# Kernel optimization log

Measured on AMD Instinct MI355X. Metric: run time of the kernel, lower is better.

Reference implementation:

```python
import jax, jax.numpy as jnp
import numpy as np

WINDOW = 127          # odd
W = (WINDOW - 1) // 2 # 63 half-window
Q_CH = WINDOW + 1     # 128 query chunk
K_CH = WINDOW * 2     # 254 key chunk


def _compl_mod(m, n):
    return int(n * int(np.ceil(m / n)) - m)


def setup_inputs() -> dict:
    key = jax.random.key(0)
    kq, kk, kv = jax.random.split(key, 3)
    B, L, NH, H = 4, 4096, 16, 64
    return {
        "q": jax.random.normal(kq, (B, L, NH, H), dtype=jnp.float32),
        "k": jax.random.normal(kk, (B, L, NH, H), dtype=jnp.float32),
        "v": jax.random.normal(kv, (B, L, NH, H), dtype=jnp.float32),
    }


def _build_mask(c, k_pad, dtype_bool=bool):
    # base band mask over one (q_ch, k_ch) block: True = masked out
    u = jnp.triu(jnp.ones((Q_CH, K_CH), dtype=bool))
    band = jnp.logical_and(u, jnp.flip(u, (0, 1)))
    base = ~band
    mask_left = base.at[:, :W].set(True)
    mask_right = base.at[:, K_CH - (W + k_pad):].set(True)
    if c > 1:
        mid = jnp.broadcast_to(base, (c - 2, Q_CH, K_CH)) if c > 2 else jnp.zeros((0, Q_CH, K_CH), bool)
        return jnp.concatenate([mask_left[None], mid, mask_right[None]], axis=0)
    return jnp.logical_or(mask_left, mask_right)[None]


def reference(q, k, v):
    b, s, nh, h = q.shape
    q = q * (h ** -0.5)

    q_pad = _compl_mod(s, Q_CH)
    k_pad = _compl_mod(s + 2 * W - K_CH, Q_CH)

    # chunk queries: (b, c, q_ch, nh, h)
    qp = jnp.pad(q, ((0, 0), (0, q_pad), (0, 0), (0, 0)))
    c = (s + q_pad) // Q_CH
    qw = qp.reshape(b, c, Q_CH, nh, h)

    # overlapping key/value windows via gather: (b, c, k_ch, nh, h)
    kp = jnp.pad(k, ((0, 0), (W, W + k_pad), (0, 0), (0, 0)))
    vp = jnp.pad(v, ((0, 0), (W, W + k_pad), (0, 0), (0, 0)))
    starts = np.arange(c) * Q_CH
    idx = starts[:, None] + np.arange(K_CH)[None, :]  # (c, k_ch)
    kw = kp[:, idx]
    vw = vp[:, idx]

    # block scores: (b, nh, c, q_ch, k_ch)
    A = jnp.einsum('bcqnh,bcknh->bncqk', qw, kw)

    mask = _build_mask(c, k_pad)  # (c, q_ch, k_ch)
    neg = -jnp.finfo(A.dtype).max
    A = jnp.where(mask[None, None], neg, A)
    A = jax.nn.softmax(A, axis=-1)

    z = jnp.einsum('bncqk,bcknh->bncqh', A, vw)  # (b, nh, c, q_ch, h)
    z = z.reshape(b, nh, c * Q_CH, h)[:, :, :s]
    return jnp.transpose(z, (0, 2, 1, 3))  # (b, s, nh, h)
```

## Files before the change

kernel.cpp:

```cpp
#include <hip/hip_runtime.h>


typedef _Float16 f16;
typedef _Float16 f16x2  __attribute__((ext_vector_type(2)));
typedef _Float16 f16x4  __attribute__((ext_vector_type(4)));
typedef _Float16 f16x8  __attribute__((ext_vector_type(8)));
typedef float    f32x16 __attribute__((ext_vector_type(16)));
typedef int      int4v  __attribute__((ext_vector_type(4)));

constexpr int NB = 4, L = 4096, NH = 16, H = 64;
constexpr int CQ = 128, NC = L / CQ, KW = 256, WR = 63;
constexpr int RS = NH * H;

constexpr int Q_OFF = 0;
constexpr int K_OFF = 16384;
constexpr int V_OFF = 49152;
constexpr int LDS_BYTES = 81920;

#define DEV static __device__ __forceinline__

DEV int iclamp(int x, int lo, int hi) { return x < lo ? lo : (x > hi ? hi : x); }

DEV float fexp2(float x) {
#if __has_builtin(__builtin_amdgcn_exp2f)
    return __builtin_amdgcn_exp2f(x);
#else
    return exp2f(x);
#endif
}

DEV int packh2(float a, float b) {
    f16x2 p; p.x = (f16)a; p.y = (f16)b;
    return __builtin_bit_cast(int, p);
}

DEV int rmaddr(int base, int r, int colb) {
    return base + r * 128 + (colb ^ ((r & 7) << 4));
}

DEV int vaddr(int h, int kb) {
    return V_OFF + ((h * 512 + kb) ^ ((((h & 7) ^ ((h >> 3) & 7))) << 4));
}

DEV int oaddr(int row, int col) {
    return (row * 64 + col) ^ ((row & 3) << 2);
}

DEV void swap_halves(int& a, int& b, int hi) {
    int pa = __shfl_xor(a, 32, 64);
    int pb = __shfl_xor(b, 32, 64);
    int na = hi ? pb : a;
    int nb = hi ? b  : pa;
    a = na; b = nb;
}

__global__ __launch_bounds__(512, 4)
void wattn_kernel(const float* __restrict__ q_, const float* __restrict__ k_,
                  const float* __restrict__ v_, float* __restrict__ o_)
{
    __shared__ alignas(16) char smem[LDS_BYTES];
    float* O_lds = (float*)smem;
    float* D_lds = (float*)(smem + 32768);

    const int bid = (int)blockIdx.x;
    const int wid = (bid & 7) * ((NB * NH * NC) / 8) + (bid >> 3);
    const int c = wid & (NC - 1);
    const int n = (wid >> 5) & (NH - 1);
    const int b = wid >> 9;

    const int t    = (int)threadIdx.x;
    const int lane = t & 63;
    const int w    = t >> 6;
    const int lq   = lane & 31;
    const int hi   = lane >> 5;
    const int qt   = w & 3;
    const int half = w >> 2;

    const int kg0 = c * CQ - WR;
    const size_t bn = ((size_t)b * L * NH + n) * H;
    const float qs = 0.125f * 1.44269504088896f;

    const int h4 = (t & 15) << 2;
    const int cb = h4 << 1;
    const int ru = t >> 4;

    {
        const float* qp = q_ + bn + (size_t)(c * CQ) * RS + h4;
        #pragma unroll
        for (int p = 0; p < 4; ++p) {
            int r = ru + p * 32;
            float4 x = *(const float4*)(qp + (size_t)r * RS);
            *(f16x4*)(smem + rmaddr(Q_OFF, r, cb)) =
                (f16x4){(f16)(x.x * qs), (f16)(x.y * qs), (f16)(x.z * qs), (f16)(x.w * qs)};
        }
    }
    #pragma unroll
    for (int p = 0; p < 8; ++p) {
        int r  = ru + p * 32;
        int kr = iclamp(kg0 + r, 0, L - 1);
        float4 x = *(const float4*)(k_ + bn + (size_t)kr * RS + h4);
        *(f16x4*)(smem + rmaddr(K_OFF, r, cb)) =
            (f16x4){(f16)x.x, (f16)x.y, (f16)x.z, (f16)x.w};
    }
    #pragma unroll
    for (int p = 0; p < 4; ++p) {
        int r0  = ru * 2 + p * 64;
        int kr0 = iclamp(kg0 + r0,     0, L - 1);
        int kr1 = iclamp(kg0 + r0 + 1, 0, L - 1);
        float4 v0 = *(const float4*)(v_ + bn + (size_t)kr0 * RS + h4);
        float4 v1 = *(const float4*)(v_ + bn + (size_t)kr1 * RS + h4);
        int kb = r0 * 2;
        *(f16x2*)(smem + vaddr(h4 + 0, kb)) = (f16x2){(f16)v0.x, (f16)v1.x};
        *(f16x2*)(smem + vaddr(h4 + 1, kb)) = (f16x2){(f16)v0.y, (f16)v1.y};
        *(f16x2*)(smem + vaddr(h4 + 2, kb)) = (f16x2){(f16)v0.z, (f16)v1.z};
        *(f16x2*)(smem + vaddr(h4 + 3, kb)) = (f16x2){(f16)v0.w, (f16)v1.w};
    }

    const int iq  = qt * 32 + lq;
    const int jlo = (c == 0) ? WR : 0;
    const int jhi = (KW < L - kg0) ? KW : (L - kg0);
    const int lo  = (iq > jlo) ? iq : jlo;
    const int hb  = (iq + 126 < jhi - 1) ? (iq + 126) : (jhi - 1);
    const unsigned span = (unsigned)(hb - lo);

    f32x16 o0, o1;
    #pragma unroll
    for (int r = 0; r < 16; ++r) { o0[r] = 0.f; o1[r] = 0.f; }
    float dsum = 0.f;

    __syncthreads();

    f16x8 qf[4];
    #pragma unroll
    for (int tq = 0; tq < 4; ++tq)
        qf[tq] = *(const f16x8*)(smem + rmaddr(Q_OFF, qt * 32 + lq, 32 * tq + 16 * hi));

    auto body = [&](int kt) {
        f16x8 kf[4];
        #pragma unroll
        for (int tq = 0; tq < 4; ++tq)
            kf[tq] = *(const f16x8*)(smem + rmaddr(K_OFF, kt * 32 + lq, 32 * tq + 16 * hi));

        f32x16 s;
        #pragma unroll
        for (int r = 0; r < 16; ++r) s[r] = 0.f;
        #pragma unroll
        for (int tq = 0; tq < 4; ++tq)
            s = __builtin_amdgcn_mfma_f32_32x32x16_f16(kf[tq], qf[tq], s, 0, 0, 0);

        const int jb = kt * 32 + 4 * hi;
        float pe[16];
        #pragma unroll
        for (int r = 0; r < 16; ++r) {
            int j = jb + (r & 3) + ((r >> 2) << 3);
            float e = fexp2(s[r]);
            e = ((unsigned)(j - lo) <= span) ? e : 0.f;
            dsum += e;
            pe[r] = e;
        }
        int d0 = packh2(pe[0],  pe[1]),  d1 = packh2(pe[2],  pe[3]);
        int d2 = packh2(pe[4],  pe[5]),  d3 = packh2(pe[6],  pe[7]);
        int d4 = packh2(pe[8],  pe[9]),  d5 = packh2(pe[10], pe[11]);
        int d6 = packh2(pe[12], pe[13]), d7 = packh2(pe[14], pe[15]);
        swap_halves(d0, d2, hi); swap_halves(d1, d3, hi);
        swap_halves(d4, d6, hi); swap_halves(d5, d7, hi);
        f16x8 pa0 = __builtin_bit_cast(f16x8, (int4v){d0, d1, d2, d3});
        f16x8 pa1 = __builtin_bit_cast(f16x8, (int4v){d4, d5, d6, d7});

        const int kb = kt * 64 + hi * 16;
        f16x8 vb00 = *(const f16x8*)(smem + vaddr(lq,      kb));
        f16x8 vb01 = *(const f16x8*)(smem + vaddr(lq,      kb + 32));
        f16x8 vb10 = *(const f16x8*)(smem + vaddr(32 + lq, kb));
        f16x8 vb11 = *(const f16x8*)(smem + vaddr(32 + lq, kb + 32));
        o0 = __builtin_amdgcn_mfma_f32_32x32x16_f16(pa0, vb00, o0, 0, 0, 0);
        o0 = __builtin_amdgcn_mfma_f32_32x32x16_f16(pa1, vb01, o0, 0, 0, 0);
        o1 = __builtin_amdgcn_mfma_f32_32x32x16_f16(pa0, vb10, o1, 0, 0, 0);
        o1 = __builtin_amdgcn_mfma_f32_32x32x16_f16(pa1, vb11, o1, 0, 0, 0);
    };

    const int kt0 = qt + half * 3;
    body(kt0);
    body(kt0 + 1);
    if (!half) body(kt0 + 2);

    float dw = dsum + __shfl_xor(dsum, 32, 64);

    __syncthreads();

    if (half) {
        #pragma unroll
        for (int r = 0; r < 16; ++r) {
            int qloc = (r & 3) + ((r >> 2) << 3) + 4 * hi;
            int row  = qt * 32 + qloc;
            O_lds[oaddr(row, lq)]      = o0[r];
            O_lds[oaddr(row, 32 + lq)] = o1[r];
        }
        if (lane < 32) D_lds[qt * 32 + lq] = dw;
    }
    __syncthreads();

    if (!half) {
        float dinv = 1.0f / (dw + D_lds[iq]);
        #pragma unroll
        for (int r = 0; r < 16; ++r) {
            int qloc = (r & 3) + ((r >> 2) << 3) + 4 * hi;
            int row  = qt * 32 + qloc;
            float rd = __shfl(dinv, qloc, 64);
            int a0 = oaddr(row, lq), a1 = oaddr(row, 32 + lq);
            O_lds[a0] = (o0[r] + O_lds[a0]) * rd;
            O_lds[a1] = (o1[r] + O_lds[a1]) * rd;
        }
    }
    __syncthreads();

    const size_t ob = ((size_t)b * L + (size_t)c * CQ) * RS + (size_t)n * H;
    #pragma unroll
    for (int it = 0; it < 4; ++it) {
        int flat = it * 512 + t;
        int row  = flat >> 4;
        int hh   = (flat & 15) << 2;
        float4 val = *(const float4*)(O_lds + oaddr(row, hh));
        *(float4*)(o_ + ob + (size_t)row * RS + hh) = val;
    }
}

extern "C" void kernel_launch(void* const* d_in, const int* in_sizes, int n_in,
                              void* d_out, int out_size, void* d_ws, size_t ws_size,
                              hipStream_t stream) {
    const float* q = (const float*)d_in[0];
    const float* k = (const float*)d_in[1];
    const float* v = (const float*)d_in[2];
    float* o = (float*)d_out;
    (void)in_sizes; (void)n_in; (void)out_size; (void)d_ws; (void)ws_size;
    wattn_kernel<<<dim3(NB * NH * NC), dim3(512), 0, stream>>>(q, k, v, o);
}
```

Baseline: 49.92 us.

## Widen global loads, use permlane32 swap, and raise wave priority around MFMA

The Q and K staging loops now load two float4 per thread (8 halves) and write f16x8 to LDS. The V transpose now packs four keys per f16x4 store, replacing f16x2 stores. The shuffle-and-select half swap of the P fragments is replaced by the single v_permlane32_swap instruction available on gfx950. s_setprio brackets the MFMA section so waves holding matrix work get scheduling priority. Together these cut instruction count in the load and exchange phases, at the cost of more registers per thread and a dependency on gfx950-specific inline asm.

```diff
diff --git a/kernel.cpp b/kernel.cpp
--- a/kernel.cpp
+++ b/kernel.cpp
@@ -2,10 +2,10 @@
 
 
 typedef _Float16 f16;
-typedef _Float16 f16x2  __attribute__((ext_vector_type(2)));
 typedef _Float16 f16x4  __attribute__((ext_vector_type(4)));
 typedef _Float16 f16x8  __attribute__((ext_vector_type(8)));
 typedef float    f32x16 __attribute__((ext_vector_type(16)));
+typedef _Float16 f16x2  __attribute__((ext_vector_type(2)));
 typedef int      int4v  __attribute__((ext_vector_type(4)));
 
 constexpr int NB = 4, L = 4096, NH = 16, H = 64;
@@ -46,12 +46,8 @@
     return (row * 64 + col) ^ ((row & 3) << 2);
 }
 
-DEV void swap_halves(int& a, int& b, int hi) {
-    int pa = __shfl_xor(a, 32, 64);
-    int pb = __shfl_xor(b, 32, 64);
-    int na = hi ? pb : a;
-    int nb = hi ? b  : pa;
-    a = na; b = nb;
+DEV void swap_halves(int& a, int& b) {
+    asm volatile("v_permlane32_swap_b32 %0, %1" : "+v"(a), "+v"(b));
 }
 
 __global__ __launch_bounds__(512, 4)
@@ -80,40 +76,44 @@
     const size_t bn = ((size_t)b * L * NH + n) * H;
     const float qs = 0.125f * 1.44269504088896f;
 
+    const int rK  = t >> 3;
+    const int hsK = (t & 7) << 3;
+    const int gV = t >> 4;
     const int h4 = (t & 15) << 2;
-    const int cb = h4 << 1;
-    const int ru = t >> 4;
-
-    {
-        const float* qp = q_ + bn + (size_t)(c * CQ) * RS + h4;
-        #pragma unroll
-        for (int p = 0; p < 4; ++p) {
-            int r = ru + p * 32;
-            float4 x = *(const float4*)(qp + (size_t)r * RS);
-            *(f16x4*)(smem + rmaddr(Q_OFF, r, cb)) =
-                (f16x4){(f16)(x.x * qs), (f16)(x.y * qs), (f16)(x.z * qs), (f16)(x.w * qs)};
-        }
-    }
-    #pragma unroll
-    for (int p = 0; p < 8; ++p) {
-        int r  = ru + p * 32;
+
+    #pragma unroll
+    for (int p = 0; p < 2; ++p) {
+        int r = rK + p * 64;
+        const float* src = q_ + bn + (size_t)(c * CQ + r) * RS + hsK;
+        float4 a = *(const float4*)(src);
+        float4 b2 = *(const float4*)(src + 4);
+        *(f16x8*)(smem + rmaddr(Q_OFF, r, hsK << 1)) =
+            (f16x8){(f16)(a.x * qs),  (f16)(a.y * qs),  (f16)(a.z * qs),  (f16)(a.w * qs),
+                    (f16)(b2.x * qs), (f16)(b2.y * qs), (f16)(b2.z * qs), (f16)(b2.w * qs)};
+    }
+    #pragma unroll
+    for (int p = 0; p < 4; ++p) {
+        int r  = rK + p * 64;
         int kr = iclamp(kg0 + r, 0, L - 1);
-        float4 x = *(const float4*)(k_ + bn + (size_t)kr * RS + h4);
-        *(f16x4*)(smem + rmaddr(K_OFF, r, cb)) =
-            (f16x4){(f16)x.x, (f16)x.y, (f16)x.z, (f16)x.w};
-    }
-    #pragma unroll
-    for (int p = 0; p < 4; ++p) {
-        int r0  = ru * 2 + p * 64;
-        int kr0 = iclamp(kg0 + r0,     0, L - 1);
-        int kr1 = iclamp(kg0 + r0 + 1, 0, L - 1);
-        float4 v0 = *(const float4*)(v_ + bn + (size_t)kr0 * RS + h4);
-        float4 v1 = *(const float4*)(v_ + bn + (size_t)kr1 * RS + h4);
-        int kb = r0 * 2;
-        *(f16x2*)(smem + vaddr(h4 + 0, kb)) = (f16x2){(f16)v0.x, (f16)v1.x};
-        *(f16x2*)(smem + vaddr(h4 + 1, kb)) = (f16x2){(f16)v0.y, (f16)v1.y};
-        *(f16x2*)(smem + vaddr(h4 + 2, kb)) = (f16x2){(f16)v0.z, (f16)v1.z};
-        *(f16x2*)(smem + vaddr(h4 + 3, kb)) = (f16x2){(f16)v0.w, (f16)v1.w};
+        const float* src = k_ + bn + (size_t)kr * RS + hsK;
+        float4 a = *(const float4*)(src);
+        float4 b2 = *(const float4*)(src + 4);
+        *(f16x8*)(smem + rmaddr(K_OFF, r, hsK << 1)) =
+            (f16x8){(f16)a.x,  (f16)a.y,  (f16)a.z,  (f16)a.w,
+                    (f16)b2.x, (f16)b2.y, (f16)b2.z, (f16)b2.w};
+    }
+    #pragma unroll
+    for (int p = 0; p < 2; ++p) {
+        int k0 = gV * 4 + p * 128;
+        float4 x0 = *(const float4*)(v_ + bn + (size_t)iclamp(kg0 + k0 + 0, 0, L - 1) * RS + h4);
+        float4 x1 = *(const float4*)(v_ + bn + (size_t)iclamp(kg0 + k0 + 1, 0, L - 1) * RS + h4);
+        float4 x2 = *(const float4*)(v_ + bn + (size_t)iclamp(kg0 + k0 + 2, 0, L - 1) * RS + h4);
+        float4 x3 = *(const float4*)(v_ + bn + (size_t)iclamp(kg0 + k0 + 3, 0, L - 1) * RS + h4);
+        int kb = k0 * 2;
+        *(f16x4*)(smem + vaddr(h4 + 0, kb)) = (f16x4){(f16)x0.x, (f16)x1.x, (f16)x2.x, (f16)x3.x};
+        *(f16x4*)(smem + vaddr(h4 + 1, kb)) = (f16x4){(f16)x0.y, (f16)x1.y, (f16)x2.y, (f16)x3.y};
+        *(f16x4*)(smem + vaddr(h4 + 2, kb)) = (f16x4){(f16)x0.z, (f16)x1.z, (f16)x2.z, (f16)x3.z};
+        *(f16x4*)(smem + vaddr(h4 + 3, kb)) = (f16x4){(f16)x0.w, (f16)x1.w, (f16)x2.w, (f16)x3.w};
     }
 
     const int iq  = qt * 32 + lq;
@@ -144,6 +144,7 @@
         f32x16 s;
         #pragma unroll
         for (int r = 0; r < 16; ++r) s[r] = 0.f;
+        __builtin_amdgcn_s_setprio(1);
         #pragma unroll
         for (int tq = 0; tq < 4; ++tq)
             s = __builtin_amdgcn_mfma_f32_32x32x16_f16(kf[tq], qf[tq], s, 0, 0, 0);
@@ -162,8 +163,8 @@
         int d2 = packh2(pe[4],  pe[5]),  d3 = packh2(pe[6],  pe[7]);
         int d4 = packh2(pe[8],  pe[9]),  d5 = packh2(pe[10], pe[11]);
         int d6 = packh2(pe[12], pe[13]), d7 = packh2(pe[14], pe[15]);
-        swap_halves(d0, d2, hi); swap_halves(d1, d3, hi);
-        swap_halves(d4, d6, hi); swap_halves(d5, d7, hi);
+        swap_halves(d0, d2); swap_halves(d1, d3);
+        swap_halves(d4, d6); swap_halves(d5, d7);
         f16x8 pa0 = __builtin_bit_cast(f16x8, (int4v){d0, d1, d2, d3});
         f16x8 pa1 = __builtin_bit_cast(f16x8, (int4v){d4, d5, d6, d7});
 
@@ -176,6 +177,7 @@
         o0 = __builtin_amdgcn_mfma_f32_32x32x16_f16(pa1, vb01, o0, 0, 0, 0);
         o1 = __builtin_amdgcn_mfma_f32_32x32x16_f16(pa0, vb10, o1, 0, 0, 0);
         o1 = __builtin_amdgcn_mfma_f32_32x32x16_f16(pa1, vb11, o1, 0, 0, 0);
+        __builtin_amdgcn_s_setprio(0);
     };
 
     const int kt0 = qt + half * 3;
```

New measurement: 54.55 us. 1.09x slower.
